# Optimization experiments

Measured on AMD Instinct MI355X. Metric: run time of the kernel, lower is better.

Reference implementation:

```python
import jax, jax.numpy as jnp
import numpy as np

B, C_IN, C_OUT, T, HID = 8, 32, 32, 8192, 64


def setup_inputs() -> dict:
    key = jax.random.key(0)
    ks = jax.random.split(key, 8)
    s1 = 1.0  # fan_in=1
    s2 = 1.0 / np.sqrt(HID)
    return {
        "x": jax.random.normal(ks[0], (B, C_IN, T), dtype=jnp.float32),
        "w1": jax.random.uniform(ks[1], (1, HID), jnp.float32, -s1, s1),
        "b1": jax.random.uniform(ks[2], (HID,), jnp.float32, -s1, s1),
        "w2": jax.random.uniform(ks[3], (HID, HID), jnp.float32, -s2, s2),
        "b2": jax.random.uniform(ks[4], (HID,), jnp.float32, -s2, s2),
        "w3": jax.random.uniform(ks[5], (HID, C_IN * C_OUT), jnp.float32, -s2, s2),
        "b3": jax.random.uniform(ks[6], (C_IN * C_OUT,), jnp.float32, -s2, s2),
        "bias": jnp.zeros((C_OUT,), dtype=jnp.float32),
    }


def _filters(w1, b1, w2, b2, w3, b3):
    # positions: (T, 1) in [0, 1]
    pos = jnp.linspace(0.0, 1.0, T, dtype=jnp.float32)[:, None]
    h = jax.nn.gelu(pos @ w1 + b1, approximate=False)
    h = jax.nn.gelu(h @ w2 + b2, approximate=False)
    f = h @ w3 + b3                      # (T, out*in)
    f = f.reshape(T, C_OUT, C_IN)
    return jnp.transpose(f, (1, 2, 0))   # (out, in, T)


def reference(x, w1, b1, w2, b2, w3, b3, bias):
    freq_x = jnp.fft.rfft(x, axis=-1)                      # (B, in, F)
    filt = _filters(w1, b1, w2, b2, w3, b3)                # (out, in, T)
    freq_f = jnp.fft.rfft(filt, axis=-1)                   # (out, in, F)
    conv_freq = jnp.einsum('bif,oif->bof', freq_x, freq_f) # contract over in
    out = jnp.fft.irfft(conv_freq, n=T, axis=-1)           # (B, out, T)
    return out + bias[None, :, None]
```

## Files before the change

### kernel.cpp

```cpp
#include <hip/hip_runtime.h>
#include <math.h>

#define T 8192
#define M 4096
#define JS 4104
#define B 8
#define CIN 32
#define COUT 32
#define HID 64
#define FT8 8

__device__ inline float2 cadd(float2 a, float2 b){ return make_float2(a.x+b.x, a.y+b.y); }
__device__ inline float2 csub(float2 a, float2 b){ return make_float2(a.x-b.x, a.y-b.y); }
__device__ inline float2 cmul(float2 a, float2 b){ return make_float2(a.x*b.x - a.y*b.y, a.x*b.y + a.y*b.x); }
__device__ inline float2 cmulc(float2 a, float2 b){
    return make_float2(a.x*b.x + a.y*b.y, a.y*b.x - a.x*b.y); }
__device__ inline float2 rot90(float2 a){ return make_float2(a.y, -a.x); }
__device__ inline int swz(int p){ return p ^ ((p >> 5) & 31); }
__device__ inline int brev12(int v){ return (int)(__brev((unsigned)v) >> 20); }

__device__ inline float2 cis_m(float k){
    const float w = -7.669903939428206e-4f;
    float a = w * k;
    return make_float2(__cosf(a), __sinf(a));
}

__device__ inline float gelu_exact(float x){
    return 0.5f*x*(1.0f + erff(x*0.70710678118654752440f));
}

template<int SH0>
__device__ inline void dif_group8_o(float2 q[8], int r){
    const float c8 = 0.70710678118654752440f;
    const float2 R8 = make_float2(c8, -c8);
    float2 b0 = cis_m((float)(r << SH0));
    float2 w0[4];
    w0[0] = b0;
    w0[1] = cmul(b0, R8);
    w0[2] = rot90(b0);
    w0[3] = rot90(w0[1]);
    {
        #pragma unroll
        for (int k = 0; k < 4; ++k){
            const int lo = k, hi = k + 4;
            float2 a = q[lo], b = q[hi];
            q[lo] = cadd(a, b);
            q[hi] = cmul(csub(a, b), w0[k]);
        }
    }
    float2 b1 = cmul(b0, b0);
    float2 w1r = rot90(b1);
    {
        #pragma unroll
        for (int k = 0; k < 4; ++k){
            const int jd = k & 1;
            const int lo = ((k & ~1) << 1) | jd, hi = lo + 2;
            float2 a = q[lo], b = q[hi];
            q[lo] = cadd(a, b);
            q[hi] = cmul(csub(a, b), jd ? w1r : b1);
        }
    }
    float2 b2 = cmul(b1, b1);
    {
        #pragma unroll
        for (int k = 0; k < 4; ++k){
            const int lo = k << 1, hi = lo + 1;
            float2 a = q[lo], b = q[hi];
            q[lo] = cadd(a, b);
            q[hi] = cmul(csub(a, b), b2);
        }
    }
}
template<int SH0>
__device__ inline void dit_group8_o(float2 q[8], int r){
    const float c8 = 0.70710678118654752440f;
    const float2 R8 = make_float2(c8, -c8);
    float2 b2 = cis_m((float)(r << (SH0-2)));
    float2 b1 = cmul(b2, b2);
    float2 b0 = cmul(b1, b1);
    {
        #pragma unroll
        for (int k = 0; k < 4; ++k){
            const int lo = k << 1, hi = lo + 1;
            float2 a = q[lo];
            float2 t2 = cmulc(q[hi], b0);
            q[lo] = cadd(a, t2);
            q[hi] = csub(a, t2);
        }
    }
    float2 w1r = rot90(b1);
    {
        #pragma unroll
        for (int k = 0; k < 4; ++k){
            const int jd = k & 1;
            const int lo = ((k & ~1) << 1) | jd, hi = lo + 2;
            float2 a = q[lo];
            float2 t2 = cmulc(q[hi], jd ? w1r : b1);
            q[lo] = cadd(a, t2);
            q[hi] = csub(a, t2);
        }
    }
    float2 w2[4];
    w2[0] = b2;
    w2[1] = cmul(b2, R8);
    w2[2] = rot90(b2);
    w2[3] = rot90(w2[1]);
    {
        #pragma unroll
        for (int k = 0; k < 4; ++k){
            const int lo = k, hi = k + 4;
            float2 a = q[lo];
            float2 t2 = cmulc(q[hi], w2[k]);
            q[lo] = cadd(a, t2);
            q[hi] = csub(a, t2);
        }
    }
}

__device__ inline void lds_store8(float2* sc, const float2* q, int base, int S){
    #pragma unroll
    for (int l = 0; l < 8; ++l) sc[swz(base + S*l)] = q[l];
}
__device__ inline void lds_load8(const float2* sc, float2* q, int base, int S){
    #pragma unroll
    for (int l = 0; l < 8; ++l) q[l] = sc[swz(base + S*l)];
}

__global__ __launch_bounds__(512) void rfft_all(const float* __restrict__ x,
        const float* __restrict__ H, float2* __restrict__ Xh, float2* __restrict__ Hh){
    __shared__ float2 sc[M];
    const int t = threadIdx.x;
    const int sig = blockIdx.x;
    const float* srow;
    float2* dp;
    if (sig < B*CIN){ srow = x + (size_t)sig*T;        dp = Xh + (size_t)sig*JS; }
    else            { srow = H + (size_t)(sig-B*CIN)*T; dp = Hh + (size_t)(sig-B*CIN)*JS; }
    const float2* zp = (const float2*)srow;
    float2 q[8];
    #pragma unroll
    for (int l = 0; l < 8; ++l) q[l] = zp[t + 512*l];
    dif_group8_o<1>(q, t);
    lds_store8(sc, q, t, 512);
    __syncthreads();
    {
        const int base = ((t>>6)<<9) | (t&63);
        lds_load8(sc, q, base, 64);
        dif_group8_o<4>(q, t&63);
        lds_store8(sc, q, base, 64);
    }
    {
        const int base = ((t>>3)<<6) | (t&7);
        lds_load8(sc, q, base, 8);
        dif_group8_o<7>(q, t&7);
        lds_store8(sc, q, base, 8);
    }
    {
        const int base = t << 3;
        lds_load8(sc, q, base, 1);
        dif_group8_o<10>(q, 0);
        lds_store8(sc, q, base, 1);
    }
    __syncthreads();
    #pragma unroll
    for (int l = 0; l < 8; ++l){
        const int j  = t + 512*l;
        const int k  = brev12(j);
        const int j2 = brev12((M - k) & (M-1));
        float2 Z  = sc[swz(j)];
        float2 Zm = sc[swz(j2)];
        float2 E = make_float2(0.5f*(Z.x + Zm.x), 0.5f*(Z.y - Zm.y));
        float2 D = make_float2(Z.x - Zm.x, Z.y + Zm.y);
        float2 O = make_float2(0.5f*D.y, -0.5f*D.x);
        float2 wk = cis_m((float)k);
        dp[j] = cadd(E, cmul(wk, O));
        if (j == 0) dp[M] = make_float2(Z.x - Z.y, 0.0f);
    }
}

__global__ __launch_bounds__(512) void irfft_out(const float2* __restrict__ Yh,
        const float* __restrict__ bias, float* __restrict__ out){
    __shared__ float2 sc[M];
    const int t = threadIdx.x;
    const int sig = blockIdx.x;
    const float2* yp = Yh + (size_t)sig*JS;
    #pragma unroll
    for (int l = 0; l < 8; ++l){
        const int j = t + 512*l;
        sc[swz(j)] = yp[j];
    }
    float2 yM = yp[M];
    __syncthreads();
    #pragma unroll
    for (int l = 0; l < 4; ++l){
        const int j = (t + 512*l) << 1;
        const int k = brev12(j);
        float2 Ym; int j2 = 0;
        if (k == 0){ Ym = yM; }
        else { j2 = brev12(M - k); Ym = sc[swz(j2)]; }
        float2 Y = sc[swz(j)];
        float2 E = make_float2(0.5f*(Y.x + Ym.x), 0.5f*(Y.y - Ym.y));
        float2 D = make_float2(0.5f*(Y.x - Ym.x), 0.5f*(Y.y + Ym.y));
        float2 wk = cis_m((float)k);
        float2 O = cmulc(D, wk);
        sc[swz(j)] = make_float2(E.x - O.y, E.y + O.x);
        if (k != 0){
            sc[swz(j2)] = make_float2(E.x + O.y, O.x - E.y);
        }
    }
    if (t == 0){
        float2 Y = sc[swz(1)];
        float2 E = make_float2(Y.x, 0.0f);
        float2 D = make_float2(0.0f, Y.y);
        float2 O = make_float2(-D.y, D.x);
        sc[swz(1)] = make_float2(E.x - O.y, E.y + O.x);
    }
    __syncthreads();
    float2 q[8];
    {
        const int base = t << 3;
        lds_load8(sc, q, base, 1);
        dit_group8_o<12>(q, 0);
        lds_store8(sc, q, base, 1);
    }
    {
        const int base = ((t>>3)<<6) | (t&7);
        lds_load8(sc, q, base, 8);
        dit_group8_o<9>(q, t&7);
        lds_store8(sc, q, base, 8);
    }
    {
        const int base = ((t>>6)<<9) | (t&63);
        lds_load8(sc, q, base, 64);
        dit_group8_o<6>(q, t&63);
        lds_store8(sc, q, base, 64);
    }
    __syncthreads();
    lds_load8(sc, q, t, 512);
    dit_group8_o<3>(q, t);
    const float scv = 1.0f/(float)M;
    const float bv = bias[sig & (COUT-1)];
    float2* op = (float2*)(out + (size_t)sig*T);
    #pragma unroll
    for (int l = 0; l < 8; ++l)
        op[t + 512*l] = make_float2(q[l].x*scv + bv, q[l].y*scv + bv);
}

#define TB 32
__global__ __launch_bounds__(256) void mlp_hidden(const float* __restrict__ w1, const float* __restrict__ b1,
                           const float* __restrict__ w2, const float* __restrict__ b2,
                           float* __restrict__ H){
    __shared__ float sw1[HID], sb1[HID], sw2[HID*HID], sb2[HID];
    __shared__ float h1s[TB][HID+1];
    const int tid = threadIdx.x;
    for (int i = tid; i < HID; i += 256){ sw1[i]=w1[i]; sb1[i]=b1[i]; sb2[i]=b2[i]; }
    for (int i = tid; i < HID*HID; i += 256) sw2[i]=w2[i];
    __syncthreads();
    const int t0 = blockIdx.x * TB;
    for (int e = tid; e < TB*HID; e += 256){
        const int tl = e & (TB-1), h = e >> 5;
        const float pos = (float)(t0 + tl) / (float)(T-1);
        h1s[tl][h] = gelu_exact(pos*sw1[h] + sb1[h]);
    }
    __syncthreads();
    const int tl = tid & (TB-1), hg = tid >> 5;
    float acc[8];
    #pragma unroll
    for (int u = 0; u < 8; ++u) acc[u] = sb2[hg*8 + u];
    for (int k = 0; k < HID; ++k){
        const float hv = h1s[tl][k];
        const float4 wa = *(const float4*)&sw2[k*HID + hg*8];
        const float4 wb = *(const float4*)&sw2[k*HID + hg*8 + 4];
        acc[0] += hv*wa.x; acc[1] += hv*wa.y; acc[2] += hv*wa.z; acc[3] += hv*wa.w;
        acc[4] += hv*wb.x; acc[5] += hv*wb.y; acc[6] += hv*wb.z; acc[7] += hv*wb.w;
    }
    #pragma unroll
    for (int u = 0; u < 8; ++u)
        H[(size_t)(hg*8 + u)*T + t0 + tl] = gelu_exact(acc[u]);
}

__global__ __launch_bounds__(256) void filt_contract(const float* __restrict__ w3,
        const float* __restrict__ b3, const float2* __restrict__ Hh,
        const float2* __restrict__ Xh, float2* __restrict__ Yh){
    __shared__ float2 Xs[CIN][73];
    __shared__ float2 Flt[16][FT8][33];
    const int t = threadIdx.x;
    const int f0 = blockIdx.y * FT8;
    const int oh = blockIdx.x;
    {
        const float4* xp4 = (const float4*)(Xh + (size_t)t*JS + f0);
        float4 u0 = xp4[0], u1 = xp4[1], u2 = xp4[2], u3 = xp4[3];
        const int b = t >> 5, i = t & 31;
        Xs[i][0*9+b] = make_float2(u0.x,u0.y); Xs[i][1*9+b] = make_float2(u0.z,u0.w);
        Xs[i][2*9+b] = make_float2(u1.x,u1.y); Xs[i][3*9+b] = make_float2(u1.z,u1.w);
        Xs[i][4*9+b] = make_float2(u2.x,u2.y); Xs[i][5*9+b] = make_float2(u2.z,u2.w);
        Xs[i][6*9+b] = make_float2(u3.x,u3.y); Xs[i][7*9+b] = make_float2(u3.z,u3.w);
    }
    const int oiG = oh*512 + (t << 1);
    float2 acc[2][FT8];
    #pragma unroll
    for (int ii = 0; ii < 2; ++ii)
        #pragma unroll
        for (int f = 0; f < FT8; ++f) acc[ii][f] = make_float2(0.f, 0.f);
    #pragma unroll 4
    for (int h = 0; h < HID; ++h){
        const float2 w2v = *(const float2*)(w3 + (size_t)h*(CIN*COUT) + oiG);
        const float4* hp4 = (const float4*)(Hh + (size_t)h*JS + f0);
        float4 a0 = hp4[0], a1 = hp4[1], a2 = hp4[2], a3 = hp4[3];
        const float hr[8] = {a0.x,a0.z,a1.x,a1.z,a2.x,a2.z,a3.x,a3.z};
        const float hi[8] = {a0.y,a0.w,a1.y,a1.w,a2.y,a2.w,a3.y,a3.w};
        const float wv[2] = {w2v.x, w2v.y};
        #pragma unroll
        for (int ii = 0; ii < 2; ++ii)
            #pragma unroll
            for (int f = 0; f < FT8; ++f){
                acc[ii][f].x += wv[ii]*hr[f];
                acc[ii][f].y += wv[ii]*hi[f];
            }
    }
    if (f0 == 0){
        #pragma unroll
        for (int ii = 0; ii < 2; ++ii)
            acc[ii][0].x += (float)T * b3[oiG + ii];
    }
    {
        const int oL = t >> 4;
        const int ib = (t & 15) << 1;
        #pragma unroll
        for (int ii = 0; ii < 2; ++ii)
            #pragma unroll
            for (int f = 0; f < FT8; ++f)
                Flt[oL][f][ib + ii] = acc[ii][f];
    }
    __syncthreads();
    const int o2 = t >> 4, f2 = (t >> 1) & 7, g = t & 1;
    float2 y[4];
    #pragma unroll
    for (int j = 0; j < 4; ++j) y[j] = make_float2(0.f, 0.f);
    #pragma unroll 8
    for (int i0 = 0; i0 < CIN; ++i0){
        const float2 fv = Flt[o2][f2][i0];
        #pragma unroll
        for (int j = 0; j < 4; ++j){
            const float2 xv = Xs[i0][f2*9 + ((g << 2) | j)];
            y[j].x += xv.x*fv.x - xv.y*fv.y;
            y[j].y += xv.x*fv.y + xv.y*fv.x;
        }
    }
    if (f0 + f2 <= M){
        #pragma unroll
        for (int j = 0; j < 4; ++j){
            const int b = (g << 2) | j;
            const int o = oh*16 + o2;
            Yh[((size_t)(b*COUT + o))*JS + f0 + f2] = y[j];
        }
    }
}

extern "C" void kernel_launch(void* const* d_in, const int* in_sizes, int n_in,
                              void* d_out, int out_size, void* d_ws, size_t ws_size,
                              hipStream_t stream){
    const float* x    = (const float*)d_in[0];
    const float* w1   = (const float*)d_in[1];
    const float* b1   = (const float*)d_in[2];
    const float* w2   = (const float*)d_in[3];
    const float* b2   = (const float*)d_in[4];
    const float* w3   = (const float*)d_in[5];
    const float* b3   = (const float*)d_in[6];
    const float* bias = (const float*)d_in[7];
    float* out = (float*)d_out;

    char* ws = (char*)d_ws;
    float2* Xh = (float2*)ws;
    float2* Yh = (float2*)(ws + (size_t)9*1024*1024);
    float2* Hh = (float2*)(ws + (size_t)18*1024*1024);
    float*  H  = (float*) (ws + (size_t)21*1024*1024);

    hipLaunchKernelGGL(mlp_hidden,    dim3(T/TB),         dim3(256), 0, stream, w1, b1, w2, b2, H);
    hipLaunchKernelGGL(rfft_all,      dim3(B*CIN+HID),    dim3(512), 0, stream, x, H, Xh, Hh);
    hipLaunchKernelGGL(filt_contract, dim3(2, M/FT8 + 1), dim3(256), 0, stream, w3, b3, Hh, Xh, Yh);
    hipLaunchKernelGGL(irfft_out,     dim3(B*COUT),       dim3(512), 0, stream, Yh, bias, out);
}
```

Before: 130.6 us.

## Fuse four kernels into one persistent kernel with grid-wide barriers

Replaces the four separate launches (MLP hidden, rfft, filter contraction, irfft) with a single 256-block persistent kernel whose phases are separated by an atomic-counter grid barrier. The blocks loop over the contraction tiles, with 512 threads each producing one output/input pair instead of two. The aim is to remove launch gaps and tail effects between stages. In exchange it adds barrier spin cost and a memset launch, and relies on all 256 blocks being co-resident, or the barrier deadlocks.

```diff
diff --git a/kernel.cpp b/kernel.cpp
--- a/kernel.cpp
+++ b/kernel.cpp
@@ -8,7 +8,8 @@
 #define CIN 32
 #define COUT 32
 #define HID 64
-#define FT8 8
+#define NB 256
+#define NT 512
 
 __device__ inline float2 cadd(float2 a, float2 b){ return make_float2(a.x+b.x, a.y+b.y); }
 __device__ inline float2 csub(float2 a, float2 b){ return make_float2(a.x-b.x, a.y-b.y); }
@@ -29,46 +30,51 @@
     return 0.5f*x*(1.0f + erff(x*0.70710678118654752440f));
 }
 
+__device__ inline void grid_sync(unsigned* bar){
+    __syncthreads();
+    __threadfence();
+    if (threadIdx.x == 0){
+        unsigned my = atomicAdd(bar, 1u);
+        unsigned target = (my/NB + 1u)*NB;
+        while (__hip_atomic_load(bar, __ATOMIC_RELAXED, __HIP_MEMORY_SCOPE_AGENT) < target){
+            __builtin_amdgcn_s_sleep(8);
+        }
+    }
+    __syncthreads();
+    __threadfence();
+}
+
 template<int SH0>
 __device__ inline void dif_group8_o(float2 q[8], int r){
     const float c8 = 0.70710678118654752440f;
     const float2 R8 = make_float2(c8, -c8);
     float2 b0 = cis_m((float)(r << SH0));
     float2 w0[4];
-    w0[0] = b0;
-    w0[1] = cmul(b0, R8);
-    w0[2] = rot90(b0);
-    w0[3] = rot90(w0[1]);
-    {
-        #pragma unroll
-        for (int k = 0; k < 4; ++k){
-            const int lo = k, hi = k + 4;
-            float2 a = q[lo], b = q[hi];
-            q[lo] = cadd(a, b);
-            q[hi] = cmul(csub(a, b), w0[k]);
-        }
+    w0[0] = b0; w0[1] = cmul(b0, R8); w0[2] = rot90(b0); w0[3] = rot90(w0[1]);
+    #pragma unroll
+    for (int k = 0; k < 4; ++k){
+        const int lo = k, hi = k + 4;
+        float2 a = q[lo], b = q[hi];
+        q[lo] = cadd(a, b);
+        q[hi] = cmul(csub(a, b), w0[k]);
     }
     float2 b1 = cmul(b0, b0);
     float2 w1r = rot90(b1);
-    {
-        #pragma unroll
-        for (int k = 0; k < 4; ++k){
-            const int jd = k & 1;
-            const int lo = ((k & ~1) << 1) | jd, hi = lo + 2;
-            float2 a = q[lo], b = q[hi];
-            q[lo] = cadd(a, b);
-            q[hi] = cmul(csub(a, b), jd ? w1r : b1);
-        }
+    #pragma unroll
+    for (int k = 0; k < 4; ++k){
+        const int jd = k & 1;
+        const int lo = ((k & ~1) << 1) | jd, hi = lo + 2;
+        float2 a = q[lo], b = q[hi];
+        q[lo] = cadd(a, b);
+        q[hi] = cmul(csub(a, b), jd ? w1r : b1);
     }
     float2 b2 = cmul(b1, b1);
-    {
-        #pragma unroll
-        for (int k = 0; k < 4; ++k){
-            const int lo = k << 1, hi = lo + 1;
-            float2 a = q[lo], b = q[hi];
-            q[lo] = cadd(a, b);
-            q[hi] = cmul(csub(a, b), b2);
-        }
+    #pragma unroll
+    for (int k = 0; k < 4; ++k){
+        const int lo = k << 1, hi = lo + 1;
+        float2 a = q[lo], b = q[hi];
+        q[lo] = cadd(a, b);
+        q[hi] = cmul(csub(a, b), b2);
     }
 }
 template<int SH0>
@@ -78,42 +84,33 @@
     float2 b2 = cis_m((float)(r << (SH0-2)));
     float2 b1 = cmul(b2, b2);
     float2 b0 = cmul(b1, b1);
-    {
-        #pragma unroll
-        for (int k = 0; k < 4; ++k){
-            const int lo = k << 1, hi = lo + 1;
-            float2 a = q[lo];
-            float2 t2 = cmulc(q[hi], b0);
-            q[lo] = cadd(a, t2);
-            q[hi] = csub(a, t2);
-        }
+    #pragma unroll
+    for (int k = 0; k < 4; ++k){
+        const int lo = k << 1, hi = lo + 1;
+        float2 a = q[lo];
+        float2 t2 = cmulc(q[hi], b0);
+        q[lo] = cadd(a, t2);
+        q[hi] = csub(a, t2);
     }
     float2 w1r = rot90(b1);
-    {
-        #pragma unroll
-        for (int k = 0; k < 4; ++k){
-            const int jd = k & 1;
-            const int lo = ((k & ~1) << 1) | jd, hi = lo + 2;
-            float2 a = q[lo];
-            float2 t2 = cmulc(q[hi], jd ? w1r : b1);
-            q[lo] = cadd(a, t2);
-            q[hi] = csub(a, t2);
-        }
+    #pragma unroll
+    for (int k = 0; k < 4; ++k){
+        const int jd = k & 1;
+        const int lo = ((k & ~1) << 1) | jd, hi = lo + 2;
+        float2 a = q[lo];
+        float2 t2 = cmulc(q[hi], jd ? w1r : b1);
+        q[lo] = cadd(a, t2);
+        q[hi] = csub(a, t2);
     }
     float2 w2[4];
-    w2[0] = b2;
-    w2[1] = cmul(b2, R8);
-    w2[2] = rot90(b2);
-    w2[3] = rot90(w2[1]);
-    {
-        #pragma unroll
-        for (int k = 0; k < 4; ++k){
-            const int lo = k, hi = k + 4;
-            float2 a = q[lo];
-            float2 t2 = cmulc(q[hi], w2[k]);
-            q[lo] = cadd(a, t2);
-            q[hi] = csub(a, t2);
-        }
+    w2[0] = b2; w2[1] = cmul(b2, R8); w2[2] = rot90(b2); w2[3] = rot90(w2[1]);
+    #pragma unroll
+    for (int k = 0; k < 4; ++k){
+        const int lo = k, hi = k + 4;
+        float2 a = q[lo];
+        float2 t2 = cmulc(q[hi], w2[k]);
+        q[lo] = cadd(a, t2);
+        q[hi] = csub(a, t2);
     }
 }
 
@@ -126,15 +123,8 @@
     for (int l = 0; l < 8; ++l) q[l] = sc[swz(base + S*l)];
 }
 
-__global__ __launch_bounds__(512) void rfft_all(const float* __restrict__ x,
-        const float* __restrict__ H, float2* __restrict__ Xh, float2* __restrict__ Hh){
-    __shared__ float2 sc[M];
-    const int t = threadIdx.x;
-    const int sig = blockIdx.x;
-    const float* srow;
-    float2* dp;
-    if (sig < B*CIN){ srow = x + (size_t)sig*T;        dp = Xh + (size_t)sig*JS; }
-    else            { srow = H + (size_t)(sig-B*CIN)*T; dp = Hh + (size_t)(sig-B*CIN)*JS; }
+__device__ void do_rfft(const float* __restrict__ srow, float2* __restrict__ dp,
+                        float2* sc, int t){
     const float2* zp = (const float2*)srow;
     float2 q[8];
     #pragma unroll
@@ -177,12 +167,8 @@
     }
 }
 
-__global__ __launch_bounds__(512) void irfft_out(const float2* __restrict__ Yh,
-        const float* __restrict__ bias, float* __restrict__ out){
-    __shared__ float2 sc[M];
-    const int t = threadIdx.x;
-    const int sig = blockIdx.x;
-    const float2* yp = Yh + (size_t)sig*JS;
+__device__ void do_irfft(const float2* __restrict__ yp, float* __restrict__ op,
+                         float bv, float2* sc, int t){
     #pragma unroll
     for (int l = 0; l < 8; ++l){
         const int j = t + 512*l;
@@ -238,121 +224,137 @@
     lds_load8(sc, q, t, 512);
     dit_group8_o<3>(q, t);
     const float scv = 1.0f/(float)M;
-    const float bv = bias[sig & (COUT-1)];
-    float2* op = (float2*)(out + (size_t)sig*T);
+    float2* o2p = (float2*)op;
     #pragma unroll
     for (int l = 0; l < 8; ++l)
-        op[t + 512*l] = make_float2(q[l].x*scv + bv, q[l].y*scv + bv);
-}
-
-#define TB 32
-__global__ __launch_bounds__(256) void mlp_hidden(const float* __restrict__ w1, const float* __restrict__ b1,
-                           const float* __restrict__ w2, const float* __restrict__ b2,
-                           float* __restrict__ H){
-    __shared__ float sw1[HID], sb1[HID], sw2[HID*HID], sb2[HID];
-    __shared__ float h1s[TB][HID+1];
-    const int tid = threadIdx.x;
-    for (int i = tid; i < HID; i += 256){ sw1[i]=w1[i]; sb1[i]=b1[i]; sb2[i]=b2[i]; }
-    for (int i = tid; i < HID*HID; i += 256) sw2[i]=w2[i];
-    __syncthreads();
-    const int t0 = blockIdx.x * TB;
-    for (int e = tid; e < TB*HID; e += 256){
-        const int tl = e & (TB-1), h = e >> 5;
-        const float pos = (float)(t0 + tl) / (float)(T-1);
-        h1s[tl][h] = gelu_exact(pos*sw1[h] + sb1[h]);
-    }
-    __syncthreads();
-    const int tl = tid & (TB-1), hg = tid >> 5;
-    float acc[8];
-    #pragma unroll
-    for (int u = 0; u < 8; ++u) acc[u] = sb2[hg*8 + u];
-    for (int k = 0; k < HID; ++k){
-        const float hv = h1s[tl][k];
-        const float4 wa = *(const float4*)&sw2[k*HID + hg*8];
-        const float4 wb = *(const float4*)&sw2[k*HID + hg*8 + 4];
-        acc[0] += hv*wa.x; acc[1] += hv*wa.y; acc[2] += hv*wa.z; acc[3] += hv*wa.w;
-        acc[4] += hv*wb.x; acc[5] += hv*wb.y; acc[6] += hv*wb.z; acc[7] += hv*wb.w;
-    }
-    #pragma unroll
-    for (int u = 0; u < 8; ++u)
-        H[(size_t)(hg*8 + u)*T + t0 + tl] = gelu_exact(acc[u]);
-}
-
-__global__ __launch_bounds__(256) void filt_contract(const float* __restrict__ w3,
-        const float* __restrict__ b3, const float2* __restrict__ Hh,
-        const float2* __restrict__ Xh, float2* __restrict__ Yh){
-    __shared__ float2 Xs[CIN][73];
-    __shared__ float2 Flt[16][FT8][33];
+        o2p[t + 512*l] = make_float2(q[l].x*scv + bv, q[l].y*scv + bv);
+}
+
+__global__ __launch_bounds__(NT) void mega(
+        const float* __restrict__ x,  const float* __restrict__ w1,
+        const float* __restrict__ b1, const float* __restrict__ w2,
+        const float* __restrict__ b2, const float* __restrict__ w3,
+        const float* __restrict__ b3, const float* __restrict__ bias,
+        float* __restrict__ out, float2* __restrict__ Xh, float2* __restrict__ Yh,
+        float2* __restrict__ Hh, float* __restrict__ H, unsigned* __restrict__ bar){
+    __shared__ __align__(16) char smem[52480];
     const int t = threadIdx.x;
-    const int f0 = blockIdx.y * FT8;
-    const int oh = blockIdx.x;
-    {
-        const float4* xp4 = (const float4*)(Xh + (size_t)t*JS + f0);
-        float4 u0 = xp4[0], u1 = xp4[1], u2 = xp4[2], u3 = xp4[3];
-        const int b = t >> 5, i = t & 31;
-        Xs[i][0*9+b] = make_float2(u0.x,u0.y); Xs[i][1*9+b] = make_float2(u0.z,u0.w);
-        Xs[i][2*9+b] = make_float2(u1.x,u1.y); Xs[i][3*9+b] = make_float2(u1.z,u1.w);
-        Xs[i][4*9+b] = make_float2(u2.x,u2.y); Xs[i][5*9+b] = make_float2(u2.z,u2.w);
-        Xs[i][6*9+b] = make_float2(u3.x,u3.y); Xs[i][7*9+b] = make_float2(u3.z,u3.w);
-    }
-    const int oiG = oh*512 + (t << 1);
-    float2 acc[2][FT8];
-    #pragma unroll
-    for (int ii = 0; ii < 2; ++ii)
+    const int blk = blockIdx.x;
+
+    {
+        float* sw1 = (float*)smem;
+        float* sb1 = sw1 + 64;
+        float* sb2 = sb1 + 64;
+        float* sw2 = sb2 + 64;
+        float* h1s = sw2 + 4096;
+        for (int i = t; i < 64; i += NT){ sw1[i]=w1[i]; sb1[i]=b1[i]; sb2[i]=b2[i]; }
+        for (int i = t; i < 4096; i += NT) sw2[i]=w2[i];
+        __syncthreads();
+        const int t0 = blk * 32;
+        for (int e = t; e < 2048; e += NT){
+            const int tl = e & 31, h = e >> 5;
+            const float pos = (float)(t0 + tl) / (float)(T-1);
+            h1s[tl*65 + h] = gelu_exact(pos*sw1[h] + sb1[h]);
+        }
+        __syncthreads();
+        const int tl = t & 31, hg = t >> 5;
+        float acc[4];
         #pragma unroll
-        for (int f = 0; f < FT8; ++f) acc[ii][f] = make_float2(0.f, 0.f);
-    #pragma unroll 4
-    for (int h = 0; h < HID; ++h){
-        const float2 w2v = *(const float2*)(w3 + (size_t)h*(CIN*COUT) + oiG);
-        const float4* hp4 = (const float4*)(Hh + (size_t)h*JS + f0);
-        float4 a0 = hp4[0], a1 = hp4[1], a2 = hp4[2], a3 = hp4[3];
-        const float hr[8] = {a0.x,a0.z,a1.x,a1.z,a2.x,a2.z,a3.x,a3.z};
-        const float hi[8] = {a0.y,a0.w,a1.y,a1.w,a2.y,a2.w,a3.y,a3.w};
-        const float wv[2] = {w2v.x, w2v.y};
+        for (int u = 0; u < 4; ++u) acc[u] = sb2[hg*4 + u];
+        for (int k = 0; k < HID; ++k){
+            const float hv = h1s[tl*65 + k];
+            const float4 w4 = *(const float4*)&sw2[k*HID + hg*4];
+            acc[0] += hv*w4.x; acc[1] += hv*w4.y; acc[2] += hv*w4.z; acc[3] += hv*w4.w;
+        }
         #pragma unroll
-        for (int ii = 0; ii < 2; ++ii)
+        for (int u = 0; u < 4; ++u)
+            H[(size_t)(hg*4 + u)*T + t0 + tl] = gelu_exact(acc[u]);
+    }
+    grid_sync(bar);
+
+    {
+        float2* sc = (float2*)smem;
+        do_rfft(x + (size_t)blk*T, Xh + (size_t)blk*JS, sc, t);
+        if (blk < HID){
+            __syncthreads();
+            do_rfft(H + (size_t)blk*T, Hh + (size_t)blk*JS, sc, t);
+        }
+    }
+    grid_sync(bar);
+
+    {
+        float2* Xs  = (float2*)smem;
+        float2* Flt = Xs + 32*73;
+        for (int tile = blk; tile < 1026; tile += NB){
+            __syncthreads();
+            const int oh = tile & 1;
+            const int f0 = (tile >> 1) * 8;
+            if (t < 256){
+                const float4* xp4 = (const float4*)(Xh + (size_t)t*JS + f0);
+                float4 u0 = xp4[0], u1 = xp4[1], u2 = xp4[2], u3 = xp4[3];
+                const int b = t >> 5, i = t & 31;
+                Xs[i*73 + 0*9 + b] = make_float2(u0.x,u0.y);
+                Xs[i*73 + 1*9 + b] = make_float2(u0.z,u0.w);
+                Xs[i*73 + 2*9 + b] = make_float2(u1.x,u1.y);
+                Xs[i*73 + 3*9 + b] = make_float2(u1.z,u1.w);
+                Xs[i*73 + 4*9 + b] = make_float2(u2.x,u2.y);
+                Xs[i*73 + 5*9 + b] = make_float2(u2.z,u2.w);
+                Xs[i*73 + 6*9 + b] = make_float2(u3.x,u3.y);
+                Xs[i*73 + 7*9 + b] = make_float2(u3.z,u3.w);
+            }
+            const int oiG = oh*512 + t;
+            float2 acc[8];
             #pragma unroll
-            for (int f = 0; f < FT8; ++f){
-                acc[ii][f].x += wv[ii]*hr[f];
-                acc[ii][f].y += wv[ii]*hi[f];
-            }
-    }
-    if (f0 == 0){
-        #pragma unroll
-        for (int ii = 0; ii < 2; ++ii)
-            acc[ii][0].x += (float)T * b3[oiG + ii];
-    }
-    {
-        const int oL = t >> 4;
-        const int ib = (t & 15) << 1;
-        #pragma unroll
-        for (int ii = 0; ii < 2; ++ii)
-            #pragma unroll
-            for (int f = 0; f < FT8; ++f)
-                Flt[oL][f][ib + ii] = acc[ii][f];
-    }
-    __syncthreads();
-    const int o2 = t >> 4, f2 = (t >> 1) & 7, g = t & 1;
-    float2 y[4];
-    #pragma unroll
-    for (int j = 0; j < 4; ++j) y[j] = make_float2(0.f, 0.f);
-    #pragma unroll 8
-    for (int i0 = 0; i0 < CIN; ++i0){
-        const float2 fv = Flt[o2][f2][i0];
-        #pragma unroll
-        for (int j = 0; j < 4; ++j){
-            const float2 xv = Xs[i0][f2*9 + ((g << 2) | j)];
-            y[j].x += xv.x*fv.x - xv.y*fv.y;
-            y[j].y += xv.x*fv.y + xv.y*fv.x;
-        }
-    }
-    if (f0 + f2 <= M){
-        #pragma unroll
-        for (int j = 0; j < 4; ++j){
-            const int b = (g << 2) | j;
-            const int o = oh*16 + o2;
-            Yh[((size_t)(b*COUT + o))*JS + f0 + f2] = y[j];
-        }
+            for (int f = 0; f < 8; ++f) acc[f] = make_float2(0.f, 0.f);
+            #pragma unroll 4
+            for (int h = 0; h < HID; ++h){
+                const float wv = w3[(size_t)h*(CIN*COUT) + oiG];
+                const float4* hp4 = (const float4*)(Hh + (size_t)h*JS + f0);
+                float4 a0 = hp4[0], a1 = hp4[1], a2 = hp4[2], a3 = hp4[3];
+                const float hr[8] = {a0.x,a0.z,a1.x,a1.z,a2.x,a2.z,a3.x,a3.z};
+                const float hi[8] = {a0.y,a0.w,a1.y,a1.w,a2.y,a2.w,a3.y,a3.w};
+                #pragma unroll
+                for (int f = 0; f < 8; ++f){
+                    acc[f].x += wv*hr[f];
+                    acc[f].y += wv*hi[f];
+                }
+            }
+            if (f0 == 0) acc[0].x += (float)T * b3[oiG];
+            {
+                const int oL = t >> 5, ii = t & 31;
+                #pragma unroll
+                for (int f = 0; f < 8; ++f)
+                    Flt[(oL*8 + f)*33 + ii] = acc[f];
+            }
+            __syncthreads();
+            const int o2 = t >> 5, f2 = (t >> 2) & 7, g = t & 3;
+            float2 y[2];
+            y[0] = make_float2(0.f, 0.f); y[1] = make_float2(0.f, 0.f);
+            #pragma unroll 8
+            for (int i0 = 0; i0 < CIN; ++i0){
+                const float2 fv = Flt[(o2*8 + f2)*33 + i0];
+                #pragma unroll
+                for (int j = 0; j < 2; ++j){
+                    const float2 xv = Xs[i0*73 + f2*9 + (4*j + g)];
+                    y[j].x += xv.x*fv.x - xv.y*fv.y;
+                    y[j].y += xv.x*fv.y + xv.y*fv.x;
+                }
+            }
+            if (f0 + f2 <= M){
+                const int o = oh*16 + o2;
+                #pragma unroll
+                for (int j = 0; j < 2; ++j){
+                    const int b = 4*j + g;
+                    Yh[((size_t)(b*COUT + o))*JS + f0 + f2] = y[j];
+                }
+            }
+        }
+    }
+    grid_sync(bar);
+
+    {
+        float2* sc = (float2*)smem;
+        do_irfft(Yh + (size_t)blk*JS, out + (size_t)blk*T, bias[blk & (COUT-1)], sc, t);
     }
 }
 
@@ -370,13 +372,13 @@
     float* out = (float*)d_out;
 
     char* ws = (char*)d_ws;
-    float2* Xh = (float2*)ws;
-    float2* Yh = (float2*)(ws + (size_t)9*1024*1024);
-    float2* Hh = (float2*)(ws + (size_t)18*1024*1024);
-    float*  H  = (float*) (ws + (size_t)21*1024*1024);
-
-    hipLaunchKernelGGL(mlp_hidden,    dim3(T/TB),         dim3(256), 0, stream, w1, b1, w2, b2, H);
-    hipLaunchKernelGGL(rfft_all,      dim3(B*CIN+HID),    dim3(512), 0, stream, x, H, Xh, Hh);
-    hipLaunchKernelGGL(filt_contract, dim3(2, M/FT8 + 1), dim3(256), 0, stream, w3, b3, Hh, Xh, Yh);
-    hipLaunchKernelGGL(irfft_out,     dim3(B*COUT),       dim3(512), 0, stream, Yh, bias, out);
-}
+    float2*  Xh  = (float2*)ws;
+    float2*  Yh  = (float2*)(ws + (size_t)9*1024*1024);
+    float2*  Hh  = (float2*)(ws + (size_t)18*1024*1024);
+    float*   H   = (float*) (ws + (size_t)21*1024*1024);
+    unsigned* bar= (unsigned*)(ws + (size_t)23*1024*1024);
+
+    hipMemsetAsync(bar, 0, 64, stream);
+    hipLaunchKernelGGL(mega, dim3(NB), dim3(NT), 0, stream,
+                       x, w1, b1, w2, b2, w3, b3, bias, out, Xh, Yh, Hh, H, bar);
+}
```

Result: slower. 433.6 us (+232.0%).
